# Kernel optimization log

Measured on AMD Instinct MI355X. Metric: run time of the kernel, lower is better.

## Reference

```python
import jax, jax.numpy as jnp
import numpy as np

B, N, D = 32, 2048, 320

def _init(key, shape, fan_in):
    return jax.random.normal(key, shape, dtype=jnp.float32) / np.sqrt(fan_in).astype(np.float32)

def setup_inputs() -> dict:
    key = jax.random.key(0)
    ks = jax.random.split(key, 11)
    return {
        "x": jax.random.normal(ks[0], (B, N, D), dtype=jnp.float32),
        # downs MLP: 320->160->80
        "W1": _init(ks[1], (320, 160), 320), "b1": jnp.zeros((160,), jnp.float32),
        "W2": _init(ks[2], (160, 80), 160),  "b2": jnp.zeros((80,), jnp.float32),
        # GraphConv1d layers: 80->40, 40->5
        "Wg1": _init(ks[3], (80, 40), 80),   "bg1": jnp.zeros((40,), jnp.float32),
        "Wg2": _init(ks[4], (40, 5), 40),    "bg2": jnp.zeros((5,), jnp.float32),
        # final classifier: 5->2
        "Wf": _init(ks[5], (5, 2), 5),       "bf": jnp.zeros((2,), jnp.float32),
    }

def _euclidean_adj(h):
    # h: [B, N, C] -> row-softmax of negative squared pairwise Euclidean distance [B, N, N]
    sq = jnp.sum(h * h, axis=-1, keepdims=True)               # [B, N, 1]
    d2 = sq - 2.0 * jnp.einsum('bnc,bmc->bnm', h, h) + jnp.swapaxes(sq, -1, -2)
    return jax.nn.softmax(-d2, axis=-1)

def _graph_conv(h, W, b):
    a = _euclidean_adj(h)                                     # dynamic adjacency
    agg = jnp.einsum('bnm,bmc->bnc', a, h)                    # neighbor aggregation
    return jax.nn.relu(agg @ W + b)

def reference(x, W1, b1, W2, b2, Wg1, bg1, Wg2, bg2, Wf, bf):
    h = jax.nn.relu(x @ W1 + b1)          # [B, N, 160]
    h = jax.nn.relu(h @ W2 + b2)          # [B, N, 80]
    h = _graph_conv(h, Wg1, bg1)          # [B, N, 40]
    h = _graph_conv(h, Wg2, bg2)          # [B, N, 5]
    h = jnp.mean(h, axis=1)               # Mean() over nodes -> [B, 5]
    logits = h @ Wf + bf                  # [B, 2]
    return jax.nn.softmax(logits, axis=-1)
```

## Files before the change

### kernel.cpp

```cpp
#include <hip/hip_runtime.h>
#include <math.h>

#define BB 32
#define NN 2048
#define D_IN 320
#define H1 160
#define H2 80
#define H4 5

typedef __attribute__((ext_vector_type(8))) short short8;
typedef __attribute__((ext_vector_type(4))) short short4v;
typedef __attribute__((ext_vector_type(4))) float f32x4;
typedef __attribute__((ext_vector_type(16))) float f32x16;

__device__ inline ushort f2bf(float f) {
    union { float f; unsigned u; } v; v.f = f;
    unsigned r = v.u + 0x7fff + ((v.u >> 16) & 1);
    return (ushort)(r >> 16);
}
__device__ inline float bf2f(ushort u) {
    union { float f; unsigned u; } v; v.u = ((unsigned)u) << 16;
    return v.f;
}
__device__ inline unsigned pkbf(float hi, float lo) {
    union { float f; unsigned u; } a, b; a.f = hi; b.f = lo;
    return __builtin_amdgcn_perm(a.u + 0x8000u, b.u + 0x8000u, 0x07060302u);
}
union U2S { unsigned u[2]; short4v s; };
union U4S { unsigned u[4]; short8 s; };

#define LOG2E  1.44269504088896340736f
#define TWOL2E 2.88539008177792681472f

__global__ __launch_bounds__(256) void prep_weights_kernel(
    const float* __restrict__ W1, const float* __restrict__ W2,
    const float* __restrict__ Wg1, const float* __restrict__ bg1,
    const float* __restrict__ Wg2, const float* __restrict__ bg2,
    ushort* __restrict__ Wt1, ushort* __restrict__ Wt2,
    ushort* __restrict__ Wg1T, float* __restrict__ bg1P,
    ushort* __restrict__ Wg2T, float* __restrict__ bg2P)
{
    const int id0 = blockIdx.x * 256 + threadIdx.x;
    const int stride = gridDim.x * 256;
    for (int i = id0; i < H1 * D_IN; i += stride) {
        const int j = i / D_IN, c = i % D_IN;
        Wt1[i] = f2bf(W1[c * H1 + j]);
    }
    for (int i = id0; i < H2 * H1; i += stride) {
        const int j = i / H1, c = i % H1;
        Wt2[i] = f2bf(W2[c * H2 + j]);
    }
    for (int i = id0; i < 64 * 96; i += stride) {
        const int j = i / 96, c = i % 96;
        Wg1T[i] = (j < 40 && c < 80) ? f2bf(Wg1[c * 40 + j]) : (ushort)0;
    }
    for (int i = id0; i < 32 * 64; i += stride) {
        const int j = i / 64, c = i % 64;
        Wg2T[i] = (j < 5 && c < 40) ? f2bf(Wg2[c * 5 + j]) : (ushort)0;
    }
    if (id0 < 64) bg1P[id0] = (id0 < 40) ? bg1[id0] : 0.f;
    if (id0 < 32) bg2P[id0] = (id0 < 5) ? bg2[id0] : 0.f;
}

__global__ __launch_bounds__(256) void mlp_mfma_kernel(
    const float* __restrict__ x,
    const ushort* __restrict__ Wt1, const float* __restrict__ b1,
    const ushort* __restrict__ Wt2, const float* __restrict__ b2,
    ushort* __restrict__ h2, ushort* __restrict__ h2T, float* __restrict__ sq2)
{
    constexpr int XST  = 72;
    constexpr int W1ST = 72;
    constexpr int H1ST = 168;

    __shared__ __attribute__((aligned(16))) ushort h1t[64 * H1ST];
    __shared__ __attribute__((aligned(16))) ushort ws1[H1 * W1ST];
    __shared__ float b1s[H1];
    __shared__ float b2s[H2];

    ushort* xs = h1t;

    const int t = threadIdx.x;
    const int lane = t & 63, w = t >> 6;
    const int colid = lane & 15, quad = lane >> 4;
    const int i = blockIdx.x;
    const int b = ((i & 7) << 2) + ((i >> 3) & 3);
    const int n0 = (i >> 5) * 64;
    const int row0 = b * NN + n0;

    if (t < H1) b1s[t] = b1[t];
    if (t < H2) b2s[t] = b2[t];

    f32x4 c1[10];
    #pragma unroll
    for (int ns = 0; ns < 10; ++ns) c1[ns] = (f32x4){0.f, 0.f, 0.f, 0.f};

    float4 xr[4];
    short8 wr[5];
    {
        #pragma unroll
        for (int i2 = 0; i2 < 4; ++i2) {
            const int id = t + i2 * 256, row = id >> 4, c4 = id & 15;
            xr[i2] = *(const float4*)&x[(size_t)(row0 + row) * D_IN + c4 * 4];
        }
        #pragma unroll
        for (int i2 = 0; i2 < 5; ++i2) {
            const int id = t + i2 * 256, j = id >> 3, part = id & 7;
            wr[i2] = *(const short8*)&Wt1[j * D_IN + part * 8];
        }
    }

    for (int kc = 0; kc < 5; ++kc) {
        if (kc) __syncthreads();
        #pragma unroll
        for (int i2 = 0; i2 < 4; ++i2) {
            const int id = t + i2 * 256, row = id >> 4, c4 = id & 15;
            uint2 up;
            up.x = pkbf(xr[i2].y, xr[i2].x);
            up.y = pkbf(xr[i2].w, xr[i2].z);
            *(uint2*)&xs[row * XST + c4 * 4] = up;
        }
        #pragma unroll
        for (int i2 = 0; i2 < 5; ++i2) {
            const int id = t + i2 * 256, j = id >> 3, part = id & 7;
            *(short8*)&ws1[j * W1ST + part * 8] = wr[i2];
        }
        __syncthreads();
        if (kc < 4) {
            const int k0 = (kc + 1) * 64;
            #pragma unroll
            for (int i2 = 0; i2 < 4; ++i2) {
                const int id = t + i2 * 256, row = id >> 4, c4 = id & 15;
                xr[i2] = *(const float4*)&x[(size_t)(row0 + row) * D_IN + k0 + c4 * 4];
            }
            #pragma unroll
            for (int i2 = 0; i2 < 5; ++i2) {
                const int id = t + i2 * 256, j = id >> 3, part = id & 7;
                wr[i2] = *(const short8*)&Wt1[j * D_IN + k0 + part * 8];
            }
        }

        short8 af[2];
        #pragma unroll
        for (int kf = 0; kf < 2; ++kf)
            af[kf] = *(const short8*)&xs[(w * 16 + colid) * XST + kf * 32 + quad * 8];
        #pragma unroll
        for (int ns = 0; ns < 10; ++ns) {
            #pragma unroll
            for (int kf = 0; kf < 2; ++kf) {
                const short8 bf = *(const short8*)&ws1[(ns * 16 + colid) * W1ST + kf * 32 + quad * 8];
                c1[ns] = __builtin_amdgcn_mfma_f32_16x16x32_bf16(af[kf], bf, c1[ns], 0, 0, 0);
            }
        }
    }
    __syncthreads();

    #pragma unroll
    for (int ns = 0; ns < 10; ++ns) {
        const float bj = b1s[ns * 16 + colid];
        #pragma unroll
        for (int r = 0; r < 4; ++r)
            h1t[(w * 16 + quad * 4 + r) * H1ST + ns * 16 + colid] =
                f2bf(fmaxf(c1[ns][r] + bj, 0.f));
    }
    __asm__ volatile("s_waitcnt lgkmcnt(0)" ::: "memory");

    short8 a2[5];
    #pragma unroll
    for (int kf = 0; kf < 5; ++kf)
        a2[kf] = *(const short8*)&h1t[(w * 16 + colid) * H1ST + kf * 32 + quad * 8];

    f32x4 c2[5];
    #pragma unroll
    for (int js = 0; js < 5; ++js) {
        f32x4 acc = (f32x4){0.f, 0.f, 0.f, 0.f};
        #pragma unroll
        for (int kf = 0; kf < 5; ++kf) {
            const short8 wb = *(const short8*)&Wt2[(js * 16 + colid) * H1 + kf * 32 + quad * 8];
            acc = __builtin_amdgcn_mfma_f32_16x16x32_bf16(a2[kf], wb, acc, 0, 0, 0);
        }
        c2[js] = acc;
    }
    __syncthreads();

    ushort* Tbuf = ws1;
    float rsq[4] = {0.f, 0.f, 0.f, 0.f};
    #pragma unroll
    for (int js = 0; js < 5; ++js) {
        const float bj = b2s[js * 16 + colid];
        #pragma unroll
        for (int r = 0; r < 4; ++r) {
            const ushort u = f2bf(fmaxf(c2[js][r] + bj, 0.f));
            const float vv = bf2f(u);
            rsq[r] += vv * vv;
            h2[(size_t)(row0 + w * 16 + quad * 4 + r) * 80 + js * 16 + colid] = u;
            Tbuf[(js * 16 + colid) * 72 + w * 16 + quad * 4 + r] = u;
        }
    }
    {
        const short8 z8 = {0, 0, 0, 0, 0, 0, 0, 0};
        const short8 ones8 = {16256, 16256, 16256, 16256, 16256, 16256, 16256, 16256};
        if (t < 128) {
            const int row = 80 + (t >> 3), part = t & 7;
            *(short8*)&Tbuf[row * 72 + part * 8] = (row == 80) ? ones8 : z8;
        }
    }
    #pragma unroll
    for (int m = 1; m <= 8; m <<= 1)
        #pragma unroll
        for (int r = 0; r < 4; ++r) rsq[r] += __shfl_xor(rsq[r], m);
    if (colid == 0) {
        #pragma unroll
        for (int r = 0; r < 4; ++r)
            sq2[(size_t)row0 + w * 16 + quad * 4 + r] = rsq[r] * LOG2E;
    }
    __syncthreads();
    for (int id = t; id < 96 * 8; id += 256) {
        const int row = id >> 3, part = id & 7;
        *(short8*)&h2T[((size_t)b * 96 + row) * NN + n0 + part * 8] =
            *(const short8*)&Tbuf[row * 72 + part * 8];
    }
}

template<int CK, int CV, int C_OUT, int JT, int ONES_CH, bool HAS_OUT, bool DO_MEAN>
__global__ __launch_bounds__(256) void attn_conv_kernel(
    const ushort* __restrict__ h, const ushort* __restrict__ hT,
    const float* __restrict__ sqg,
    const ushort* __restrict__ WtG, const float* __restrict__ biasP,
    ushort* __restrict__ ho, ushort* __restrict__ hoT, float* __restrict__ sqo,
    float* __restrict__ mean_out)
{
    constexpr int CF   = CK / 16;
    constexpr int CFP  = CV / 16;
    constexpr int CSV  = CV / 32;
    constexpr int KST  = CK + 8;
    constexpr int VST  = 64 + 8;
    constexpr int KPR  = CK / 8;
    constexpr int KTOT = 64 * KPR;
    constexpr int NK   = (KTOT + 255) / 256;
    constexpr int NV   = (CV * 8) / 256;
    constexpr int TST  = 136;
    constexpr int CS1  = ONES_CH / 32;
    constexpr int R1   = ((ONES_CH % 32) / 8) * 4 + (ONES_CH & 3);
    constexpr int LDSN = 64 * KST + CV * VST;

    __shared__ __attribute__((aligned(16))) ushort ldsbuf[LDSN];
    __shared__ __attribute__((aligned(16))) float sqs[64];
    ushort* Krow = ldsbuf;
    ushort* Vcol = ldsbuf + 64 * KST;

    const int t = threadIdx.x;
    const int lane = t & 63, w = t >> 6;
    const int m32 = lane & 31, hl = lane >> 5;
    const int i = blockIdx.x;
    const int b = ((i & 7) << 2) + ((i >> 3) & 3);
    const int n0blk = (i >> 5) * 128;
    const int qrow = n0blk + w * 32 + m32;

    short8 qf[CF];
    {
        const ushort* qr = h + ((size_t)b * NN + qrow) * CK;
        #pragma unroll
        for (int c = 0; c < CF; ++c)
            qf[c] = *(const short8*)&qr[c * 16 + hl * 8];
    }
    const float nsqnQL = -sqg[(size_t)b * NN + qrow];

    f32x16 o[CSV];
    #pragma unroll
    for (int cs = 0; cs < CSV; ++cs)
        #pragma unroll
        for (int r = 0; r < 16; ++r) o[cs][r] = 0.f;

    short8 kreg[NK], vreg[NV];
    float sqreg = 0.f;
    {
        const ushort* hsrc = h + (size_t)((size_t)b * NN) * CK;
        #pragma unroll
        for (int i2 = 0; i2 < NK; ++i2) {
            const int id = t + i2 * 256;
            if (KTOT % 256 == 0 || id < KTOT)
                kreg[i2] = *(const short8*)&hsrc[id * 8];
        }
        #pragma unroll
        for (int i2 = 0; i2 < NV; ++i2) {
            const int id = t + i2 * 256, c = id >> 3, pt = id & 7;
            vreg[i2] = *(const short8*)&hT[((size_t)b * CV + c) * NN + pt * 8];
        }
        if (t < 64) sqreg = sqg[(size_t)b * NN + t];
    }

    for (int n0 = 0; n0 < NN; n0 += 64) {
        if (n0) __syncthreads();
        #pragma unroll
        for (int i2 = 0; i2 < NK; ++i2) {
            const int id = t + i2 * 256;
            if (KTOT % 256 == 0 || id < KTOT) {
                const int row = id / KPR, pt = id % KPR;
                *(short8*)&Krow[row * KST + pt * 8] = kreg[i2];
            }
        }
        #pragma unroll
        for (int i2 = 0; i2 < NV; ++i2) {
            const int id = t + i2 * 256, c = id >> 3, pt = id & 7;
            *(short8*)&Vcol[c * VST + pt * 8] = vreg[i2];
        }
        if (t < 64) sqs[t] = sqreg;
        __syncthreads();
        if (n0 + 64 < NN) {
            const int n1 = n0 + 64;
            const ushort* hsrc = h + (size_t)((size_t)b * NN + n1) * CK;
            #pragma unroll
            for (int i2 = 0; i2 < NK; ++i2) {
                const int id = t + i2 * 256;
                if (KTOT % 256 == 0 || id < KTOT)
                    kreg[i2] = *(const short8*)&hsrc[id * 8];
            }
            #pragma unroll
            for (int i2 = 0; i2 < NV; ++i2) {
                const int id = t + i2 * 256, c = id >> 3, pt = id & 7;
                vreg[i2] = *(const short8*)&hT[((size_t)b * CV + c) * NN + n1 + pt * 8];
            }
            if (t < 64) sqreg = sqg[(size_t)b * NN + n1 + t];
        }

        #pragma unroll
        for (int T = 0; T < 2; ++T) {
            f32x16 st;
            #pragma unroll
            for (int r = 0; r < 16; ++r) st[r] = 0.f;
            #pragma unroll
            for (int c = 0; c < CF; ++c) {
                const short8 af = *(const short8*)&Krow[(T * 32 + m32) * KST + c * 16 + hl * 8];
                st = __builtin_amdgcn_mfma_f32_32x32x16_bf16(af, qf[c], st, 0, 0, 0);
            }
            float p[16];
            #pragma unroll
            for (int g = 0; g < 4; ++g) {
                const f32x4 smv = *(const f32x4*)&sqs[T * 32 + g * 8 + hl * 4];
                #pragma unroll
                for (int r2 = 0; r2 < 4; ++r2)
                    p[g * 4 + r2] = exp2f(fmaf(st[g * 4 + r2], TWOL2E,
                                               nsqnQL - smv[r2]));
            }
            #pragma unroll
            for (int c = 0; c < 2; ++c) {
                U4S pk_;
                #pragma unroll
                for (int bq = 0; bq < 4; ++bq)
                    pk_.u[bq] = pkbf(p[c * 8 + bq * 2 + 1], p[c * 8 + bq * 2]);
                const int kb = (T * 2 + c) * 16 + hl * 4;
                #pragma unroll
                for (int cs = 0; cs < CSV; ++cs) {
                    U4S va;
                    *(short4v*)&va.u[0] = *(const short4v*)&Vcol[(cs * 32 + m32) * VST + kb];
                    *(short4v*)&va.u[2] = *(const short4v*)&Vcol[(cs * 32 + m32) * VST + kb + 8];
                    o[cs] = __builtin_amdgcn_mfma_f32_32x32x16_bf16(va.s, pk_.s, o[cs], 0, 0, 0);
                }
            }
        }
    }
    __syncthreads();

    float rsv = (hl == 0) ? o[CS1][R1] : 0.f;
    rsv += __shfl_xor(rsv, 32);
    const float rinv = 1.f / rsv;

    short8 ob[CFP];
    #pragma unroll
    for (int cs = 0; cs < CSV; ++cs)
        #pragma unroll
        for (int c2 = 0; c2 < 2; ++c2) {
            U4S ob_;
            #pragma unroll
            for (int bq = 0; bq < 4; ++bq)
                ob_.u[bq] = pkbf(o[cs][c2 * 8 + bq * 2 + 1] * rinv,
                                 o[cs][c2 * 8 + bq * 2] * rinv);
            ob[cs * 2 + c2] = ob_.s;
        }

    ushort* Tbuf = ldsbuf;
    float rsq = 0.f;
    float msum[4] = {0.f, 0.f, 0.f, 0.f};

    #pragma unroll
    for (int jt = 0; jt < JT; ++jt) {
        f32x16 acc;
        #pragma unroll
        for (int r = 0; r < 16; ++r) acc[r] = 0.f;
        #pragma unroll
        for (int cc = 0; cc < CFP; ++cc) {
            const ushort* wrow = WtG + (size_t)(jt * 32 + m32) * CV + cc * 16 + hl * 4;
            U4S wa;
            *(short4v*)&wa.u[0] = *(const short4v*)&wrow[0];
            *(short4v*)&wa.u[2] = *(const short4v*)&wrow[8];
            acc = __builtin_amdgcn_mfma_f32_32x32x16_bf16(wa.s, ob[cc], acc, 0, 0, 0);
        }
        #pragma unroll
        for (int g = 0; g < 4; ++g) {
            const f32x4 bv = *(const f32x4*)&biasP[jt * 32 + g * 8 + hl * 4];
            float v[4];
            #pragma unroll
            for (int r2 = 0; r2 < 4; ++r2) {
                v[r2] = fmaxf(acc[g * 4 + r2] + bv[r2], 0.f);
                rsq += v[r2] * v[r2];
            }
            if (HAS_OUT) {
                U2S uo;
                uo.u[0] = pkbf(v[1], v[0]);
                uo.u[1] = pkbf(v[3], v[2]);
                const int jb = jt * 32 + g * 8 + hl * 4;
                if (jb < 48)
                    *(short4v*)&ho[((size_t)b * NN + qrow) * 48 + jb] = uo.s;
                const int qc = w * 32 + m32;
                #pragma unroll
                for (int r2 = 0; r2 < 4; ++r2)
                    Tbuf[(jb + r2) * TST + qc] =
                        (ushort)(uo.u[r2 >> 1] >> ((r2 & 1) * 16));
            }
            if (DO_MEAN && jt == 0 && g == 0) {
                #pragma unroll
                for (int r2 = 0; r2 < 4; ++r2) msum[r2] = v[r2];
            }
        }
    }

    if (HAS_OUT) {
        const float rsq2 = rsq + __shfl_xor(rsq, 32);
        if (hl == 0) sqo[(size_t)b * NN + qrow] = rsq2 * LOG2E;
        __syncthreads();
        const short8 ones8 = {16256, 16256, 16256, 16256, 16256, 16256, 16256, 16256};
        for (int id = t; id < 64 * 16; id += 256) {
            const int row = id >> 4, part = id & 15;
            const short8 val = (row == 40) ? ones8
                             : *(const short8*)&Tbuf[row * TST + part * 8];
            *(short8*)&hoT[((size_t)b * 64 + row) * NN + n0blk + part * 8] = val;
        }
    }
    if (DO_MEAN) {
        #pragma unroll
        for (int s = 1; s <= 16; s <<= 1)
            #pragma unroll
            for (int r2 = 0; r2 < 4; ++r2) msum[r2] += __shfl_xor(msum[r2], s);
        if (m32 == 0) {
            if (hl == 0) {
                #pragma unroll
                for (int r2 = 0; r2 < 4; ++r2)
                    atomicAdd(&mean_out[b * C_OUT + r2], msum[r2] * (1.f / NN));
            } else {
                atomicAdd(&mean_out[b * C_OUT + 4], msum[0] * (1.f / NN));
            }
        }
    }
}

__global__ __launch_bounds__(64) void final_kernel(
    const float* __restrict__ mean, const float* __restrict__ Wf,
    const float* __restrict__ bf, float* __restrict__ out)
{
    const int t = threadIdx.x;
    const int b = t >> 1, k = t & 1;
    float acc = bf[k];
    #pragma unroll
    for (int c = 0; c < H4; ++c) acc += mean[b * H4 + c] * Wf[c * 2 + k];
    const float other = __shfl_xor(acc, 1);
    const float mx = fmaxf(acc, other);
    const float e  = __expf(acc - mx);
    const float eo = __expf(other - mx);
    out[t] = e / (e + eo);
}

extern "C" void kernel_launch(void* const* d_in, const int* in_sizes, int n_in,
                              void* d_out, int out_size, void* d_ws, size_t ws_size,
                              hipStream_t stream) {
    const float* x   = (const float*)d_in[0];
    const float* W1  = (const float*)d_in[1];
    const float* b1  = (const float*)d_in[2];
    const float* W2  = (const float*)d_in[3];
    const float* b2  = (const float*)d_in[4];
    const float* Wg1 = (const float*)d_in[5];
    const float* bg1 = (const float*)d_in[6];
    const float* Wg2 = (const float*)d_in[7];
    const float* bg2 = (const float*)d_in[8];
    const float* Wf  = (const float*)d_in[9];
    const float* bf  = (const float*)d_in[10];

    ushort* h2   = (ushort*)d_ws;
    ushort* h2T  = h2  + (size_t)BB * NN * 80;
    float*  sq2  = (float*)(h2T + (size_t)BB * 96 * NN);
    ushort* h3   = (ushort*)(sq2 + (size_t)BB * NN);
    ushort* h3T  = h3  + (size_t)BB * NN * 48;
    float*  sq3  = (float*)(h3T + (size_t)BB * 64 * NN);
    float*  meanb = sq3 + (size_t)BB * NN;
    ushort* Wt1  = (ushort*)(meanb + 160);
    ushort* Wt2  = Wt1 + (size_t)H1 * D_IN;
    ushort* Wg1T = Wt2 + (size_t)H2 * H1;
    float*  bg1P = (float*)(Wg1T + 64 * 96);
    ushort* Wg2T = (ushort*)(bg1P + 64);
    float*  bg2P = (float*)(Wg2T + 32 * 64);

    hipMemsetAsync(meanb, 0, BB * H4 * sizeof(float), stream);

    prep_weights_kernel<<<64, 256, 0, stream>>>(W1, W2, Wg1, bg1, Wg2, bg2,
                                                Wt1, Wt2, Wg1T, bg1P, Wg2T, bg2P);
    mlp_mfma_kernel<<<BB * NN / 64, 256, 0, stream>>>(x, Wt1, b1, Wt2, b2, h2, h2T, sq2);
    attn_conv_kernel<80, 96, 40, 2, 80, true,  false><<<BB * NN / 128, 256, 0, stream>>>(
        h2, h2T, sq2, Wg1T, bg1P, h3, h3T, sq3, nullptr);
    attn_conv_kernel<48, 64, 5, 1, 40, false, true><<<BB * NN / 128, 256, 0, stream>>>(
        h3, h3T, sq3, Wg2T, bg2P, nullptr, nullptr, nullptr, meanb);
    final_kernel<<<1, 64, 0, stream>>>(meanb, Wf, bf, (float*)d_out);
}
```

Baseline: 310.4 us.

## Double-buffer K/V tiles in LDS and permute V/weight layout for single wide loads

Replaces the single LDS K/V buffer with two buffers, so the next tile is staged into the other buffer while the current one is consumed. This leaves one barrier per iteration and lets global loads run two tiles ahead. V columns and the graph-conv weights are stored in a permuted k-order, so each MFMA operand becomes one 16-byte LDS or global read instead of two 8-byte reads. LDS use doubles, which may lower occupancy, and the permutation has to match the MFMA operand layout exactly.

```diff
diff --git a/kernel.cpp b/kernel.cpp
--- a/kernel.cpp
+++ b/kernel.cpp
@@ -27,7 +27,7 @@
     return __builtin_amdgcn_perm(a.u + 0x8000u, b.u + 0x8000u, 0x07060302u);
 }
 union U2S { unsigned u[2]; short4v s; };
-union U4S { unsigned u[4]; short8 s; };
+union U4S { unsigned u[4]; short8 s; short4v h[2]; };
 
 #define LOG2E  1.44269504088896340736f
 #define TWOL2E 2.88539008177792681472f
@@ -52,11 +52,15 @@
     }
     for (int i = id0; i < 64 * 96; i += stride) {
         const int j = i / 96, c = i % 96;
-        Wg1T[i] = (j < 40 && c < 80) ? f2bf(Wg1[c * 40 + j]) : (ushort)0;
+        const int c4 = c & 15;
+        const int pos = (c & ~15) + (c4 & 3) + (((c4 >> 3) & 1) << 2) + (((c4 >> 2) & 1) << 3);
+        Wg1T[j * 96 + pos] = (j < 40 && c < 80) ? f2bf(Wg1[c * 40 + j]) : (ushort)0;
     }
     for (int i = id0; i < 32 * 64; i += stride) {
         const int j = i / 64, c = i % 64;
-        Wg2T[i] = (j < 5 && c < 40) ? f2bf(Wg2[c * 5 + j]) : (ushort)0;
+        const int c4 = c & 15;
+        const int pos = (c & ~15) + (c4 & 3) + (((c4 >> 3) & 1) << 2) + (((c4 >> 2) & 1) << 3);
+        Wg2T[j * 64 + pos] = (j < 5 && c < 40) ? f2bf(Wg2[c * 5 + j]) : (ushort)0;
     }
     if (id0 < 64) bg1P[id0] = (id0 < 40) ? bg1[id0] : 0.f;
     if (id0 < 32) bg2P[id0] = (id0 < 5) ? bg2[id0] : 0.f;
@@ -229,8 +233,8 @@
     ushort* __restrict__ ho, ushort* __restrict__ hoT, float* __restrict__ sqo,
     float* __restrict__ mean_out)
 {
+    constexpr int CFP  = CV / 16;
     constexpr int CF   = CK / 16;
-    constexpr int CFP  = CV / 16;
     constexpr int CSV  = CV / 32;
     constexpr int KST  = CK + 8;
     constexpr int VST  = 64 + 8;
@@ -241,12 +245,10 @@
     constexpr int TST  = 136;
     constexpr int CS1  = ONES_CH / 32;
     constexpr int R1   = ((ONES_CH % 32) / 8) * 4 + (ONES_CH & 3);
-    constexpr int LDSN = 64 * KST + CV * VST;
-
-    __shared__ __attribute__((aligned(16))) ushort ldsbuf[LDSN];
-    __shared__ __attribute__((aligned(16))) float sqs[64];
-    ushort* Krow = ldsbuf;
-    ushort* Vcol = ldsbuf + 64 * KST;
+    constexpr int BUFN = 64 * KST + CV * VST;
+
+    __shared__ __attribute__((aligned(16))) ushort ldsbuf[2][BUFN];
+    __shared__ __attribute__((aligned(16))) float sqs[2][64];
 
     const int t = threadIdx.x;
     const int lane = t & 63, w = t >> 6;
@@ -273,8 +275,9 @@
 
     short8 kreg[NK], vreg[NV];
     float sqreg = 0.f;
-    {
-        const ushort* hsrc = h + (size_t)((size_t)b * NN) * CK;
+
+    auto loadTile = [&](int n1) {
+        const ushort* hsrc = h + ((size_t)b * NN + n1) * CK;
         #pragma unroll
         for (int i2 = 0; i2 < NK; ++i2) {
             const int id = t + i2 * 256;
@@ -284,44 +287,45 @@
         #pragma unroll
         for (int i2 = 0; i2 < NV; ++i2) {
             const int id = t + i2 * 256, c = id >> 3, pt = id & 7;
-            vreg[i2] = *(const short8*)&hT[((size_t)b * CV + c) * NN + pt * 8];
-        }
-        if (t < 64) sqreg = sqg[(size_t)b * NN + t];
-    }
-
-    for (int n0 = 0; n0 < NN; n0 += 64) {
-        if (n0) __syncthreads();
+            vreg[i2] = *(const short8*)&hT[((size_t)b * CV + c) * NN + n1 + pt * 8];
+        }
+        if (t < 64) sqreg = sqg[(size_t)b * NN + n1 + t];
+    };
+    auto stageTile = [&](int buf) {
+        ushort* Kd = ldsbuf[buf];
+        ushort* Vd = ldsbuf[buf] + 64 * KST;
         #pragma unroll
         for (int i2 = 0; i2 < NK; ++i2) {
             const int id = t + i2 * 256;
             if (KTOT % 256 == 0 || id < KTOT) {
                 const int row = id / KPR, pt = id % KPR;
-                *(short8*)&Krow[row * KST + pt * 8] = kreg[i2];
+                *(short8*)&Kd[row * KST + pt * 8] = kreg[i2];
             }
         }
         #pragma unroll
         for (int i2 = 0; i2 < NV; ++i2) {
             const int id = t + i2 * 256, c = id >> 3, pt = id & 7;
-            *(short8*)&Vcol[c * VST + pt * 8] = vreg[i2];
-        }
-        if (t < 64) sqs[t] = sqreg;
-        __syncthreads();
-        if (n0 + 64 < NN) {
-            const int n1 = n0 + 64;
-            const ushort* hsrc = h + (size_t)((size_t)b * NN + n1) * CK;
-            #pragma unroll
-            for (int i2 = 0; i2 < NK; ++i2) {
-                const int id = t + i2 * 256;
-                if (KTOT % 256 == 0 || id < KTOT)
-                    kreg[i2] = *(const short8*)&hsrc[id * 8];
-            }
-            #pragma unroll
-            for (int i2 = 0; i2 < NV; ++i2) {
-                const int id = t + i2 * 256, c = id >> 3, pt = id & 7;
-                vreg[i2] = *(const short8*)&hT[((size_t)b * CV + c) * NN + n1 + pt * 8];
-            }
-            if (t < 64) sqreg = sqg[(size_t)b * NN + n1 + t];
-        }
+            const int colb = ((pt >> 1) << 4) + ((pt & 1) << 2);
+            U4S vv; vv.s = vreg[i2];
+            *(short4v*)&Vd[c * VST + colb]     = vv.h[0];
+            *(short4v*)&Vd[c * VST + colb + 8] = vv.h[1];
+        }
+        if (t < 64) sqs[buf][t] = sqreg;
+    };
+
+    loadTile(0);
+    stageTile(0);
+    __syncthreads();
+    loadTile(64);
+
+    for (int it = 0; it < NN / 64; ++it) {
+        const int cur = it & 1;
+        if (it + 1 < NN / 64) {
+            stageTile(cur ^ 1);
+            if (it + 2 < NN / 64) loadTile((it + 2) * 64);
+        }
+        const ushort* Krow = ldsbuf[cur];
+        const ushort* Vcol = ldsbuf[cur] + 64 * KST;
 
         #pragma unroll
         for (int T = 0; T < 2; ++T) {
@@ -336,7 +340,7 @@
             float p[16];
             #pragma unroll
             for (int g = 0; g < 4; ++g) {
-                const f32x4 smv = *(const f32x4*)&sqs[T * 32 + g * 8 + hl * 4];
+                const f32x4 smv = *(const f32x4*)&sqs[cur][T * 32 + g * 8 + hl * 4];
                 #pragma unroll
                 for (int r2 = 0; r2 < 4; ++r2)
                     p[g * 4 + r2] = exp2f(fmaf(st[g * 4 + r2], TWOL2E,
@@ -348,18 +352,16 @@
                 #pragma unroll
                 for (int bq = 0; bq < 4; ++bq)
                     pk_.u[bq] = pkbf(p[c * 8 + bq * 2 + 1], p[c * 8 + bq * 2]);
-                const int kb = (T * 2 + c) * 16 + hl * 4;
+                const int kb = (T * 2 + c) * 16 + hl * 8;
                 #pragma unroll
                 for (int cs = 0; cs < CSV; ++cs) {
-                    U4S va;
-                    *(short4v*)&va.u[0] = *(const short4v*)&Vcol[(cs * 32 + m32) * VST + kb];
-                    *(short4v*)&va.u[2] = *(const short4v*)&Vcol[(cs * 32 + m32) * VST + kb + 8];
-                    o[cs] = __builtin_amdgcn_mfma_f32_32x32x16_bf16(va.s, pk_.s, o[cs], 0, 0, 0);
+                    const short8 va = *(const short8*)&Vcol[(cs * 32 + m32) * VST + kb];
+                    o[cs] = __builtin_amdgcn_mfma_f32_32x32x16_bf16(va, pk_.s, o[cs], 0, 0, 0);
                 }
             }
         }
-    }
-    __syncthreads();
+        __syncthreads();
+    }
 
     float rsv = (hl == 0) ? o[CS1][R1] : 0.f;
     rsv += __shfl_xor(rsv, 32);
@@ -378,7 +380,7 @@
             ob[cs * 2 + c2] = ob_.s;
         }
 
-    ushort* Tbuf = ldsbuf;
+    ushort* Tbuf = (ushort*)ldsbuf;
     float rsq = 0.f;
     float msum[4] = {0.f, 0.f, 0.f, 0.f};
 
@@ -389,11 +391,8 @@
         for (int r = 0; r < 16; ++r) acc[r] = 0.f;
         #pragma unroll
         for (int cc = 0; cc < CFP; ++cc) {
-            const ushort* wrow = WtG + (size_t)(jt * 32 + m32) * CV + cc * 16 + hl * 4;
-            U4S wa;
-            *(short4v*)&wa.u[0] = *(const short4v*)&wrow[0];
-            *(short4v*)&wa.u[2] = *(const short4v*)&wrow[8];
-            acc = __builtin_amdgcn_mfma_f32_32x32x16_bf16(wa.s, ob[cc], acc, 0, 0, 0);
+            const short8 wa = *(const short8*)&WtG[(size_t)(jt * 32 + m32) * CV + cc * 16 + hl * 8];
+            acc = __builtin_amdgcn_mfma_f32_32x32x16_bf16(wa, ob[cc], acc, 0, 0, 0);
         }
         #pragma unroll
         for (int g = 0; g < 4; ++g) {
```

Result: no change. 316.1 us (+1.8%).
